# Kernel tuning notes

Measured on AMD Instinct MI355X. Metric: run time of the kernel, lower is better.

## Reference

```python
import jax, jax.numpy as jnp
import numpy as np

B, T, D, H = 2, 2048, 1024, 16
DH = D // H  # head_dim = 64
ROPE_BASE = 10000.0


def _rope_cos_sin(seq_len, dh, dtype):
    inv_freq = 1.0 / (ROPE_BASE ** (jnp.arange(0, dh, 2, dtype=jnp.float32) / dh))
    t = jnp.arange(seq_len, dtype=jnp.float32)
    freqs = jnp.outer(t, inv_freq)            # [T, dh/2]
    emb = jnp.concatenate([freqs, freqs], -1)  # [T, dh]
    return jnp.cos(emb).astype(dtype), jnp.sin(emb).astype(dtype)


def _rotate_half(x):
    half = x.shape[-1] // 2
    return jnp.concatenate([-x[..., half:], x[..., :half]], axis=-1)


def setup_inputs() -> dict:
    key = jax.random.key(0)
    k1, k2, k3 = jax.random.split(key, 3)
    x = jax.random.normal(k1, (B, T, D), dtype=jnp.float32)
    w_qkv = jax.random.normal(k2, (D, 3 * D), dtype=jnp.float32) * (D ** -0.5)
    w_out = jax.random.normal(k3, (D, D), dtype=jnp.float32) * (D ** -0.5)
    return {"x": x, "w_qkv": w_qkv, "w_out": w_out}


def reference(x, w_qkv, w_out):
    b, t, _ = x.shape
    qkv = x @ w_qkv                                        # [B,T,3D]
    qkv = qkv.reshape(b, t, 3, H, DH).transpose(2, 0, 3, 1, 4)  # [3,B,H,T,DH]
    q, k, v = qkv[0], qkv[1], qkv[2]

    cos, sin = _rope_cos_sin(t, DH, x.dtype)               # [T,DH] each
    q = q * cos + _rotate_half(q) * sin
    k = k * cos + _rotate_half(k) * sin

    scale = DH ** -0.5
    scores = jnp.einsum('bhtd,bhsd->bhts', q, k) * scale   # [B,H,T,T]
    # dense additive causal mask (as in original module)
    neg = jnp.finfo(x.dtype).min
    causal = jnp.triu(jnp.ones((t, t), dtype=bool), k=1)
    scores = scores + jnp.where(causal, neg, jnp.zeros((), x.dtype))
    attn = jax.nn.softmax(scores, axis=-1)
    out = jnp.einsum('bhts,bhsd->bhtd', attn, v)           # [B,H,T,DH]
    out = out.transpose(0, 2, 1, 3).reshape(b, t, D)       # [B,T,D]
    return out @ w_out
```

## Files before the change

### kernel.cpp

```cpp
#include <hip/hip_runtime.h>

typedef __bf16 bf16x8 __attribute__((ext_vector_type(8)));
typedef float f32x4 __attribute__((ext_vector_type(4)));
typedef unsigned int u32x4 __attribute__((ext_vector_type(4)));
typedef unsigned int u32x2 __attribute__((ext_vector_type(2)));
typedef unsigned short u16;
typedef unsigned int u32;

#define BSZ 2
#define TSEQ 2048
#define DMODEL 1024
#define NHEAD 16
#define DHEAD 64

#define GLDS(gp, lp)                                                        \
  __builtin_amdgcn_global_load_lds(                                         \
      (const __attribute__((address_space(1))) void*)(gp),                  \
      (__attribute__((address_space(3))) void*)(lp), 16, 0, 0)

#define TRR(dst, base, OFF)                                                 \
  asm volatile("ds_read_b64_tr_b16 %0, %1 offset:" OFF                     \
               : "=v"(dst) : "v"(base) : "memory")

__device__ __forceinline__ u16 f2bf(float f) {
  return __builtin_bit_cast(u16, (__bf16)f);
}
__device__ __forceinline__ float bf2f(u16 h) {
  return __builtin_bit_cast(float, (u32)h << 16);
}

__global__ void k_cvt(const float* __restrict__ in, u16* __restrict__ out, int n4) {
  int i = blockIdx.x * 256 + threadIdx.x;
  if (i >= n4) return;
  float4 v = ((const float4*)in)[i];
  ushort4 o;
  o.x = f2bf(v.x); o.y = f2bf(v.y); o.z = f2bf(v.z); o.w = f2bf(v.w);
  ((ushort4*)out)[i] = o;
}

__global__ void k_transpose_cvt(const float* __restrict__ in, u16* __restrict__ out,
                                int K, int N) {
  __shared__ float tile[64][65];
  int n0 = blockIdx.x * 64, k0 = blockIdx.y * 64;
  int tx = threadIdx.x & 63, ty = threadIdx.x >> 6;
#pragma unroll
  for (int i = ty; i < 64; i += 4)
    tile[i][tx] = in[(size_t)(k0 + i) * N + n0 + tx];
  __syncthreads();
#pragma unroll
  for (int i = ty; i < 64; i += 4)
    out[(size_t)(n0 + i) * K + k0 + tx] = f2bf(tile[tx][i]);
}

__global__ void k_rope_table(float* __restrict__ cosT, float* __restrict__ sinT) {
  int idx = blockIdx.x * 256 + threadIdx.x;
  int t = idx >> 5, f = idx & 31;
  float inv_freq = powf(10000.0f, -(float)(2 * f) / 64.0f);
  float ang = (float)t * inv_freq;
  float s, c;
  sincosf(ang, &s, &c);
  cosT[idx] = c;
  sinT[idx] = s;
}

template <typename OutT>
__global__ __launch_bounds__(256) void k_gemm(const u16* __restrict__ A,
                                              const u16* __restrict__ Bt,
                                              OutT* __restrict__ C, int M, int N, int K) {
  __shared__ __align__(16) u16 a_lds[2][128][32];
  __shared__ __align__(16) u16 b_lds[2][128][32];
  int m0 = blockIdx.y * 128, n0 = blockIdx.x * 128;
  int tid = threadIdx.x;
  int w = tid >> 6, l = tid & 63, lr = l & 15, lg = l >> 4;
  int wr = (w >> 1) * 64, wc = (w & 1) * 64;
  int grow = l >> 2;
  int gcol = (l & 3) * 8;
  f32x4 acc[4][4] = {};

  const u16* a0 = A + (size_t)(m0 + w * 16 + grow) * K + gcol;
  const u16* a1 = A + (size_t)(m0 + (w + 4) * 16 + grow) * K + gcol;
  const u16* b0 = Bt + (size_t)(n0 + w * 16 + grow) * K + gcol;
  const u16* b1 = Bt + (size_t)(n0 + (w + 4) * 16 + grow) * K + gcol;

  int NT = K >> 5;
  GLDS(a0, &a_lds[0][w * 16][0]);
  GLDS(a1, &a_lds[0][(w + 4) * 16][0]);
  GLDS(b0, &b_lds[0][w * 16][0]);
  GLDS(b1, &b_lds[0][(w + 4) * 16][0]);

  for (int t = 0; t < NT; ++t) {
    int p = t & 1;
    if (t + 1 < NT) {
      int k0 = (t + 1) << 5;
      GLDS(a0 + k0, &a_lds[p ^ 1][w * 16][0]);
      GLDS(a1 + k0, &a_lds[p ^ 1][(w + 4) * 16][0]);
      GLDS(b0 + k0, &b_lds[p ^ 1][w * 16][0]);
      GLDS(b1 + k0, &b_lds[p ^ 1][(w + 4) * 16][0]);
      asm volatile("s_waitcnt vmcnt(4)" ::: "memory");
    } else {
      asm volatile("s_waitcnt vmcnt(0)" ::: "memory");
    }
    __builtin_amdgcn_s_barrier();
    __builtin_amdgcn_sched_barrier(0);
    bf16x8 af[4], bfv[4];
#pragma unroll
    for (int mt = 0; mt < 4; ++mt)
      af[mt] = __builtin_bit_cast(bf16x8, *(const u32x4*)&a_lds[p][wr + mt * 16 + lr][lg * 8]);
#pragma unroll
    for (int nt = 0; nt < 4; ++nt)
      bfv[nt] = __builtin_bit_cast(bf16x8, *(const u32x4*)&b_lds[p][wc + nt * 16 + lr][lg * 8]);
    __builtin_amdgcn_s_setprio(1);
#pragma unroll
    for (int mt = 0; mt < 4; ++mt)
#pragma unroll
      for (int nt = 0; nt < 4; ++nt)
        acc[mt][nt] = __builtin_amdgcn_mfma_f32_16x16x32_bf16(af[mt], bfv[nt], acc[mt][nt], 0, 0, 0);
    __builtin_amdgcn_s_setprio(0);
    __builtin_amdgcn_sched_barrier(0);
    __builtin_amdgcn_s_barrier();
  }

#pragma unroll
  for (int mt = 0; mt < 4; ++mt)
#pragma unroll
    for (int nt = 0; nt < 4; ++nt)
#pragma unroll
      for (int r = 0; r < 4; ++r) {
        int row = m0 + wr + mt * 16 + lg * 4 + r;
        int col = n0 + wc + nt * 16 + lr;
        C[(size_t)row * N + col] = acc[mt][nt][r];
      }
}

__global__ __launch_bounds__(256) void k_gemm_qkv(const u16* __restrict__ A,
                                                  const u16* __restrict__ Bt,
                                                  u16* __restrict__ Qh, u16* __restrict__ Kh,
                                                  u16* __restrict__ Vh,
                                                  const float* __restrict__ cosT,
                                                  const float* __restrict__ sinT) {
  const int M = BSZ * TSEQ, N = 3 * DMODEL, K = DMODEL;
  __shared__ __align__(16) u16 a_lds[2][128][32];
  __shared__ __align__(16) u16 b_lds[2][128][32];
  int m0 = blockIdx.y * 128, n0 = blockIdx.x * 128;
  int tid = threadIdx.x;
  int w = tid >> 6, l = tid & 63, lr = l & 15, lg = l >> 4;
  int wr = (w >> 1) * 64, wc = (w & 1) * 64;
  int grow = l >> 2;
  int gcol = (l & 3) * 8;
  f32x4 acc[4][4] = {};

  const u16* a0 = A + (size_t)(m0 + w * 16 + grow) * K + gcol;
  const u16* a1 = A + (size_t)(m0 + (w + 4) * 16 + grow) * K + gcol;
  const u16* b0 = Bt + (size_t)(n0 + w * 16 + grow) * K + gcol;
  const u16* b1 = Bt + (size_t)(n0 + (w + 4) * 16 + grow) * K + gcol;

  int NT = K >> 5;
  GLDS(a0, &a_lds[0][w * 16][0]);
  GLDS(a1, &a_lds[0][(w + 4) * 16][0]);
  GLDS(b0, &b_lds[0][w * 16][0]);
  GLDS(b1, &b_lds[0][(w + 4) * 16][0]);

  for (int t = 0; t < NT; ++t) {
    int p = t & 1;
    if (t + 1 < NT) {
      int k0 = (t + 1) << 5;
      GLDS(a0 + k0, &a_lds[p ^ 1][w * 16][0]);
      GLDS(a1 + k0, &a_lds[p ^ 1][(w + 4) * 16][0]);
      GLDS(b0 + k0, &b_lds[p ^ 1][w * 16][0]);
      GLDS(b1 + k0, &b_lds[p ^ 1][(w + 4) * 16][0]);
      asm volatile("s_waitcnt vmcnt(4)" ::: "memory");
    } else {
      asm volatile("s_waitcnt vmcnt(0)" ::: "memory");
    }
    __builtin_amdgcn_s_barrier();
    __builtin_amdgcn_sched_barrier(0);
    bf16x8 af[4], bfv[4];
#pragma unroll
    for (int mt = 0; mt < 4; ++mt)
      af[mt] = __builtin_bit_cast(bf16x8, *(const u32x4*)&a_lds[p][wr + mt * 16 + lr][lg * 8]);
#pragma unroll
    for (int nt = 0; nt < 4; ++nt)
      bfv[nt] = __builtin_bit_cast(bf16x8, *(const u32x4*)&b_lds[p][wc + nt * 16 + lr][lg * 8]);
    __builtin_amdgcn_s_setprio(1);
#pragma unroll
    for (int mt = 0; mt < 4; ++mt)
#pragma unroll
      for (int nt = 0; nt < 4; ++nt)
        acc[mt][nt] = __builtin_amdgcn_mfma_f32_16x16x32_bf16(af[mt], bfv[nt], acc[mt][nt], 0, 0, 0);
    __builtin_amdgcn_s_setprio(0);
    __builtin_amdgcn_sched_barrier(0);
    __builtin_amdgcn_s_barrier();
  }

  int sec = n0 >> 10;
  int hcol = ((n0 + wc) & 1023) >> 6;
  u16* outp = (sec == 0) ? Qh : (sec == 1) ? Kh : Vh;
  float qscale = (sec == 0) ? 0.125f : 1.0f;
#pragma unroll
  for (int mt = 0; mt < 4; ++mt)
#pragma unroll
    for (int r = 0; r < 4; ++r) {
      int row = m0 + wr + mt * 16 + lg * 4 + r;
      int b = row >> 11, tt = row & 2047;
      size_t obase = ((size_t)((b * 16 + hcol) * 2048 + tt)) * 64;
      if (sec == 2) {
#pragma unroll
        for (int nt = 0; nt < 4; ++nt)
          outp[obase + nt * 16 + lr] = f2bf(acc[mt][nt][r]);
      } else {
        float c0 = cosT[tt * 32 + lr],      s0 = sinT[tt * 32 + lr];
        float c1 = cosT[tt * 32 + 16 + lr], s1 = sinT[tt * 32 + 16 + lr];
        float v0 = acc[mt][0][r], v1 = acc[mt][1][r];
        float v2 = acc[mt][2][r], v3 = acc[mt][3][r];
        outp[obase + lr]      = f2bf((v0 * c0 - v2 * s0) * qscale);
        outp[obase + 16 + lr] = f2bf((v1 * c1 - v3 * s1) * qscale);
        outp[obase + 32 + lr] = f2bf((v2 * c0 + v0 * s0) * qscale);
        outp[obase + 48 + lr] = f2bf((v3 * c1 + v1 * s1) * qscale);
      }
    }
}

__global__ __launch_bounds__(256) void k_flash(const u16* __restrict__ Qg, const u16* __restrict__ Kg,
                                               const u16* __restrict__ Vg, u16* __restrict__ O) {
  __shared__ __align__(16) u16 k_lds[2][64][72];
  __shared__ __align__(16) u16 vsub[2][4096];
  __shared__ __align__(16) u16 p_lds[4][16][68];
  int pairIdx = blockIdx.x;
  int bh = blockIdx.y;
  int b = bh >> 4, h = bh & 15;
  size_t hoff = (size_t)bh * TSEQ * DHEAD;
  int tid = threadIdx.x, w = tid >> 6, l = tid & 63, lr = l & 15, lg = l >> 4;

  int srow = tid >> 3;
  int g8 = tid & 7;
  int sc8 = g8 * 8;
  u32 vtr0 = (u32)(uintptr_t)vsub + (u32)(lg * 1024 + lr * 8);

  const u16* kbase = Kg + hoff;
  const u16* vbase = Vg + hoff;

  for (int sub = 0; sub < 2; ++sub) {
    int qb = sub == 0 ? (31 - pairIdx) : pairIdx;

    int qrow = qb * 64 + w * 16 + lr;
    const u16* qp = Qg + hoff + (size_t)qrow * 64 + lg * 8;
    bf16x8 qf0 = __builtin_bit_cast(bf16x8, *(const u32x4*)qp);
    bf16x8 qf1 = __builtin_bit_cast(bf16x8, *(const u32x4*)(qp + 32));

    f32x4 acc[4] = {};
    float mrow[4] = {-1e30f, -1e30f, -1e30f, -1e30f};
    float lrow[4] = {0.f, 0.f, 0.f, 0.f};

    u32x4 kreg[2], vreg[2];
#pragma unroll
    for (int p = 0; p < 2; ++p) {
      int r = srow + p * 32;
      kreg[p] = *(const u32x4*)(kbase + (size_t)r * 64 + sc8);
      vreg[p] = *(const u32x4*)(vbase + (size_t)r * 64 + sc8);
    }
    __syncthreads();

    for (int kv = 0; kv <= qb; ++kv) {
      int cur = kv & 1;
#pragma unroll
      for (int p = 0; p < 2; ++p) {
        int r = srow + p * 32;
        *(u32x4*)&k_lds[cur][r][sc8] = kreg[p];
        int vo = ((r >> 2) * 4 + (g8 >> 1)) * 64 + (r & 3) * 16 + (g8 & 1) * 8;
        *(u32x4*)&vsub[cur][vo] = vreg[p];
      }
      __syncthreads();
      if (kv < qb) {
#pragma unroll
        for (int p = 0; p < 2; ++p) {
          int r = (kv + 1) * 64 + srow + p * 32;
          kreg[p] = *(const u32x4*)(kbase + (size_t)r * 64 + sc8);
          vreg[p] = *(const u32x4*)(vbase + (size_t)r * 64 + sc8);
        }
      }

      f32x4 s[4];
      __builtin_amdgcn_s_setprio(1);
#pragma unroll
      for (int c = 0; c < 4; ++c) {
        const u16* kp2 = &k_lds[cur][c * 16 + lr][lg * 8];
        bf16x8 kf0 = __builtin_bit_cast(bf16x8, *(const u32x4*)kp2);
        bf16x8 kf1 = __builtin_bit_cast(bf16x8, *(const u32x4*)(kp2 + 32));
        f32x4 z = {};
        z = __builtin_amdgcn_mfma_f32_16x16x32_bf16(qf0, kf0, z, 0, 0, 0);
        s[c] = __builtin_amdgcn_mfma_f32_16x16x32_bf16(qf1, kf1, z, 0, 0, 0);
      }
      __builtin_amdgcn_s_setprio(0);
      if (kv == qb) {
#pragma unroll
        for (int c = 0; c < 4; ++c)
#pragma unroll
          for (int r = 0; r < 4; ++r)
            if (c * 16 + lr > w * 16 + lg * 4 + r) s[c][r] = -1e30f;
      }

      float rmax[4];
#pragma unroll
      for (int r = 0; r < 4; ++r)
        rmax[r] = fmaxf(fmaxf(s[0][r], s[1][r]), fmaxf(s[2][r], s[3][r]));
#pragma unroll
      for (int mset = 1; mset <= 8; mset <<= 1)
#pragma unroll
        for (int r = 0; r < 4; ++r)
          rmax[r] = fmaxf(rmax[r], __shfl_xor(rmax[r], mset, 64));
      bool need = (rmax[0] > mrow[0] + 8.0f) | (rmax[1] > mrow[1] + 8.0f) |
                  (rmax[2] > mrow[2] + 8.0f) | (rmax[3] > mrow[3] + 8.0f);
      if (__any(need)) {
        float alpha[4];
#pragma unroll
        for (int r = 0; r < 4; ++r) {
          float mn = fmaxf(mrow[r], rmax[r]);
          alpha[r] = __expf(mrow[r] - mn);
          mrow[r] = mn;
          lrow[r] *= alpha[r];
        }
#pragma unroll
        for (int n = 0; n < 4; ++n)
#pragma unroll
          for (int r = 0; r < 4; ++r)
            acc[n][r] *= alpha[r];
      }
#pragma unroll
      for (int c = 0; c < 4; ++c)
#pragma unroll
        for (int r = 0; r < 4; ++r) {
          float pe = __expf(s[c][r] - mrow[r]);
          s[c][r] = pe;
          lrow[r] += pe;
        }

#pragma unroll
      for (int c = 0; c < 4; ++c)
#pragma unroll
        for (int r = 0; r < 4; ++r)
          p_lds[w][lg * 4 + r][c * 16 + lr] = f2bf(s[c][r]);
      bf16x8 pa0 = __builtin_bit_cast(bf16x8, *(const u32x4*)&p_lds[w][lr][lg * 8]);
      bf16x8 pa1 = __builtin_bit_cast(bf16x8, *(const u32x4*)&p_lds[w][lr][lg * 8 + 32]);

      u32 vtr = vtr0 + (u32)(cur * 8192);
      {
        u32x2 t[8];
        TRR(t[0], vtr, "0");    TRR(t[1], vtr, "512");
        TRR(t[2], vtr, "4096"); TRR(t[3], vtr, "4608");
        TRR(t[4], vtr, "128");  TRR(t[5], vtr, "640");
        TRR(t[6], vtr, "4224"); TRR(t[7], vtr, "4736");
        asm volatile("s_waitcnt lgkmcnt(0)" ::: "memory");
        __builtin_amdgcn_sched_barrier(0);
        __builtin_amdgcn_s_setprio(1);
#pragma unroll
        for (int n2 = 0; n2 < 2; ++n2) {
          u32x4 vlo, vhi;
          vlo[0] = t[n2 * 4 + 0][0]; vlo[1] = t[n2 * 4 + 0][1];
          vlo[2] = t[n2 * 4 + 1][0]; vlo[3] = t[n2 * 4 + 1][1];
          vhi[0] = t[n2 * 4 + 2][0]; vhi[1] = t[n2 * 4 + 2][1];
          vhi[2] = t[n2 * 4 + 3][0]; vhi[3] = t[n2 * 4 + 3][1];
          acc[n2] = __builtin_amdgcn_mfma_f32_16x16x32_bf16(pa0, __builtin_bit_cast(bf16x8, vlo), acc[n2], 0, 0, 0);
          acc[n2] = __builtin_amdgcn_mfma_f32_16x16x32_bf16(pa1, __builtin_bit_cast(bf16x8, vhi), acc[n2], 0, 0, 0);
        }
        __builtin_amdgcn_s_setprio(0);
      }
      {
        u32x2 t[8];
        TRR(t[0], vtr, "256");  TRR(t[1], vtr, "768");
        TRR(t[2], vtr, "4352"); TRR(t[3], vtr, "4864");
        TRR(t[4], vtr, "384");  TRR(t[5], vtr, "896");
        TRR(t[6], vtr, "4480"); TRR(t[7], vtr, "4992");
        asm volatile("s_waitcnt lgkmcnt(0)" ::: "memory");
        __builtin_amdgcn_sched_barrier(0);
        __builtin_amdgcn_s_setprio(1);
#pragma unroll
        for (int n2 = 0; n2 < 2; ++n2) {
          int n = 2 + n2;
          u32x4 vlo, vhi;
          vlo[0] = t[n2 * 4 + 0][0]; vlo[1] = t[n2 * 4 + 0][1];
          vlo[2] = t[n2 * 4 + 1][0]; vlo[3] = t[n2 * 4 + 1][1];
          vhi[0] = t[n2 * 4 + 2][0]; vhi[1] = t[n2 * 4 + 2][1];
          vhi[2] = t[n2 * 4 + 3][0]; vhi[3] = t[n2 * 4 + 3][1];
          acc[n] = __builtin_amdgcn_mfma_f32_16x16x32_bf16(pa0, __builtin_bit_cast(bf16x8, vlo), acc[n], 0, 0, 0);
          acc[n] = __builtin_amdgcn_mfma_f32_16x16x32_bf16(pa1, __builtin_bit_cast(bf16x8, vhi), acc[n], 0, 0, 0);
        }
        __builtin_amdgcn_s_setprio(0);
      }
    }

#pragma unroll
    for (int mset = 1; mset <= 8; mset <<= 1)
#pragma unroll
      for (int r = 0; r < 4; ++r)
        lrow[r] += __shfl_xor(lrow[r], mset, 64);
#pragma unroll
    for (int n = 0; n < 4; ++n)
#pragma unroll
      for (int r = 0; r < 4; ++r) {
        int t = qb * 64 + w * 16 + lg * 4 + r;
        int dd = n * 16 + lr;
        float ov = acc[n][r] / lrow[r];
        O[(size_t)(b * TSEQ + t) * DMODEL + h * 64 + dd] = f2bf(ov);
      }
  }
}

extern "C" void kernel_launch(void* const* d_in, const int* in_sizes, int n_in,
                              void* d_out, int out_size, void* d_ws, size_t ws_size,
                              hipStream_t stream) {
  const float* x     = (const float*)d_in[0];
  const float* w_qkv = (const float*)d_in[1];
  const float* w_out = (const float*)d_in[2];
  float* out = (float*)d_out;

  char* ws = (char*)d_ws;
  size_t off = 0;
  auto alloc = [&](size_t bytes) {
    char* p = ws + off;
    off += (bytes + 255) & ~(size_t)255;
    return p;
  };
  const size_t MT = (size_t)BSZ * TSEQ;
  u16* xb    = (u16*)alloc(MT * DMODEL * 2);
  u16* wqkvT = (u16*)alloc((size_t)3 * DMODEL * DMODEL * 2);
  u16* woutT = (u16*)alloc((size_t)DMODEL * DMODEL * 2);
  u16* Qh    = (u16*)alloc(MT * DMODEL * 2);
  u16* Kh    = (u16*)alloc(MT * DMODEL * 2);
  u16* Vh    = (u16*)alloc(MT * DMODEL * 2);
  u16* aout  = (u16*)alloc(MT * DMODEL * 2);
  float* cosT = (float*)alloc((size_t)TSEQ * 32 * 4);
  float* sinT = (float*)alloc((size_t)TSEQ * 32 * 4);
  if (ws_size < off) return;

  k_cvt<<<(MT * DMODEL / 4 + 255) / 256, 256, 0, stream>>>(x, xb, MT * DMODEL / 4);
  k_transpose_cvt<<<dim3(48, 16), 256, 0, stream>>>(w_qkv, wqkvT, DMODEL, 3 * DMODEL);
  k_transpose_cvt<<<dim3(16, 16), 256, 0, stream>>>(w_out, woutT, DMODEL, DMODEL);
  k_rope_table<<<(TSEQ * 32) / 256, 256, 0, stream>>>(cosT, sinT);
  k_gemm_qkv<<<dim3(24, 32), 256, 0, stream>>>(xb, wqkvT, Qh, Kh, Vh, cosT, sinT);
  k_flash<<<dim3(16, BSZ * NHEAD), 256, 0, stream>>>(Qh, Kh, Vh, aout);
  k_gemm<float><<<dim3(8, 32), 256, 0, stream>>>(aout, woutT, out, (int)MT, DMODEL, DMODEL);
}
```

Measured before the change: 218.2 us.

## Merge prep kernels, run both causal query blocks concurrently, shrink output GEMM tile

The four preprocessing kernels (x convert, two weight transposes, rope table) are merged into one launch to cut launch overhead. The flash kernel now uses 512 threads, with two 4-wave teams each handling one query block of the balanced pair at the same time over a shared K/V stream, instead of processing the pair one after the other. The output projection gets its own kernel with 128x64 tiles, doubling the number of blocks so the GPU is better filled. Costs: more LDS and registers per flash block, and the team with the shorter query block sits idle during the later KV iterations while still joining the barriers.

```diff
diff --git a/kernel.cpp b/kernel.cpp
--- a/kernel.cpp
+++ b/kernel.cpp
@@ -25,48 +25,68 @@
 __device__ __forceinline__ u16 f2bf(float f) {
   return __builtin_bit_cast(u16, (__bf16)f);
 }
+__device__ __forceinline__ u32 pack2bf(float lo, float hi) {
+  return (u32)f2bf(lo) | ((u32)f2bf(hi) << 16);
+}
 __device__ __forceinline__ float bf2f(u16 h) {
   return __builtin_bit_cast(float, (u32)h << 16);
 }
 
-__global__ void k_cvt(const float* __restrict__ in, u16* __restrict__ out, int n4) {
-  int i = blockIdx.x * 256 + threadIdx.x;
-  if (i >= n4) return;
-  float4 v = ((const float4*)in)[i];
-  ushort4 o;
-  o.x = f2bf(v.x); o.y = f2bf(v.y); o.z = f2bf(v.z); o.w = f2bf(v.w);
-  ((ushort4*)out)[i] = o;
-}
-
-__global__ void k_transpose_cvt(const float* __restrict__ in, u16* __restrict__ out,
-                                int K, int N) {
+__global__ void k_prep(const float* __restrict__ x, u16* __restrict__ xb,
+                       const float* __restrict__ wqkv, u16* __restrict__ wqkvT,
+                       const float* __restrict__ wout, u16* __restrict__ woutT,
+                       float* __restrict__ cosT, float* __restrict__ sinT) {
   __shared__ float tile[64][65];
-  int n0 = blockIdx.x * 64, k0 = blockIdx.y * 64;
-  int tx = threadIdx.x & 63, ty = threadIdx.x >> 6;
-#pragma unroll
-  for (int i = ty; i < 64; i += 4)
-    tile[i][tx] = in[(size_t)(k0 + i) * N + n0 + tx];
-  __syncthreads();
-#pragma unroll
-  for (int i = ty; i < 64; i += 4)
-    out[(size_t)(n0 + i) * K + k0 + tx] = f2bf(tile[tx][i]);
-}
-
-__global__ void k_rope_table(float* __restrict__ cosT, float* __restrict__ sinT) {
-  int idx = blockIdx.x * 256 + threadIdx.x;
-  int t = idx >> 5, f = idx & 31;
-  float inv_freq = powf(10000.0f, -(float)(2 * f) / 64.0f);
-  float ang = (float)t * inv_freq;
-  float s, c;
-  sincosf(ang, &s, &c);
-  cosT[idx] = c;
-  sinT[idx] = s;
-}
-
-template <typename OutT>
-__global__ __launch_bounds__(256) void k_gemm(const u16* __restrict__ A,
-                                              const u16* __restrict__ Bt,
-                                              OutT* __restrict__ C, int M, int N, int K) {
+  int blk = blockIdx.x, tid = threadIdx.x;
+  if (blk < 2048) {
+    int i = blk * 256 + tid;
+    const float4* f4 = (const float4*)x;
+    float4 v0 = f4[i * 2], v1 = f4[i * 2 + 1];
+    u32x4 o;
+    o[0] = pack2bf(v0.x, v0.y); o[1] = pack2bf(v0.z, v0.w);
+    o[2] = pack2bf(v1.x, v1.y); o[3] = pack2bf(v1.z, v1.w);
+    ((u32x4*)xb)[i] = o;
+  } else if (blk < 2816) {
+    int idx = blk - 2048;
+    int n0 = (idx % 48) * 64, k0 = (idx / 48) * 64;
+    int tx = tid & 63, ty = tid >> 6;
+#pragma unroll
+    for (int i = ty; i < 64; i += 4)
+      tile[i][tx] = wqkv[(size_t)(k0 + i) * 3072 + n0 + tx];
+    __syncthreads();
+#pragma unroll
+    for (int i = ty; i < 64; i += 4)
+      wqkvT[(size_t)(n0 + i) * 1024 + k0 + tx] = f2bf(tile[tx][i]);
+  } else if (blk < 3072) {
+    int idx = blk - 2816;
+    int n0 = (idx % 16) * 64, k0 = (idx / 16) * 64;
+    int tx = tid & 63, ty = tid >> 6;
+#pragma unroll
+    for (int i = ty; i < 64; i += 4)
+      tile[i][tx] = wout[(size_t)(k0 + i) * 1024 + n0 + tx];
+    __syncthreads();
+#pragma unroll
+    for (int i = ty; i < 64; i += 4)
+      woutT[(size_t)(n0 + i) * 1024 + k0 + tx] = f2bf(tile[tx][i]);
+  } else {
+    int idx = (blk - 3072) * 256 + tid;
+    int t = idx >> 5, f = idx & 31;
+    float inv_freq = powf(10000.0f, -(float)(2 * f) / 64.0f);
+    float ang = (float)t * inv_freq;
+    float s, c;
+    sincosf(ang, &s, &c);
+    cosT[idx] = c;
+    sinT[idx] = s;
+  }
+}
+
+__global__ __launch_bounds__(256) void k_gemm_qkv(const u16* __restrict__ A,
+                                                  const u16* __restrict__ Bt,
+                                                  u16* __restrict__ Qh, u16* __restrict__ Kh,
+                                                  u16* __restrict__ Vh,
+                                                  const float* __restrict__ cosT,
+                                                  const float* __restrict__ sinT) {
+  const int K = DMODEL;
   __shared__ __align__(16) u16 a_lds[2][128][32];
   __shared__ __align__(16) u16 b_lds[2][128][32];
   int m0 = blockIdx.y * 128, n0 = blockIdx.x * 128;
@@ -120,78 +140,6 @@
     __builtin_amdgcn_s_barrier();
   }
 
-#pragma unroll
-  for (int mt = 0; mt < 4; ++mt)
-#pragma unroll
-    for (int nt = 0; nt < 4; ++nt)
-#pragma unroll
-      for (int r = 0; r < 4; ++r) {
-        int row = m0 + wr + mt * 16 + lg * 4 + r;
-        int col = n0 + wc + nt * 16 + lr;
-        C[(size_t)row * N + col] = acc[mt][nt][r];
-      }
-}
-
-__global__ __launch_bounds__(256) void k_gemm_qkv(const u16* __restrict__ A,
-                                                  const u16* __restrict__ Bt,
-                                                  u16* __restrict__ Qh, u16* __restrict__ Kh,
-                                                  u16* __restrict__ Vh,
-                                                  const float* __restrict__ cosT,
-                                                  const float* __restrict__ sinT) {
-  const int M = BSZ * TSEQ, N = 3 * DMODEL, K = DMODEL;
-  __shared__ __align__(16) u16 a_lds[2][128][32];
-  __shared__ __align__(16) u16 b_lds[2][128][32];
-  int m0 = blockIdx.y * 128, n0 = blockIdx.x * 128;
-  int tid = threadIdx.x;
-  int w = tid >> 6, l = tid & 63, lr = l & 15, lg = l >> 4;
-  int wr = (w >> 1) * 64, wc = (w & 1) * 64;
-  int grow = l >> 2;
-  int gcol = (l & 3) * 8;
-  f32x4 acc[4][4] = {};
-
-  const u16* a0 = A + (size_t)(m0 + w * 16 + grow) * K + gcol;
-  const u16* a1 = A + (size_t)(m0 + (w + 4) * 16 + grow) * K + gcol;
-  const u16* b0 = Bt + (size_t)(n0 + w * 16 + grow) * K + gcol;
-  const u16* b1 = Bt + (size_t)(n0 + (w + 4) * 16 + grow) * K + gcol;
-
-  int NT = K >> 5;
-  GLDS(a0, &a_lds[0][w * 16][0]);
-  GLDS(a1, &a_lds[0][(w + 4) * 16][0]);
-  GLDS(b0, &b_lds[0][w * 16][0]);
-  GLDS(b1, &b_lds[0][(w + 4) * 16][0]);
-
-  for (int t = 0; t < NT; ++t) {
-    int p = t & 1;
-    if (t + 1 < NT) {
-      int k0 = (t + 1) << 5;
-      GLDS(a0 + k0, &a_lds[p ^ 1][w * 16][0]);
-      GLDS(a1 + k0, &a_lds[p ^ 1][(w + 4) * 16][0]);
-      GLDS(b0 + k0, &b_lds[p ^ 1][w * 16][0]);
-      GLDS(b1 + k0, &b_lds[p ^ 1][(w + 4) * 16][0]);
-      asm volatile("s_waitcnt vmcnt(4)" ::: "memory");
-    } else {
-      asm volatile("s_waitcnt vmcnt(0)" ::: "memory");
-    }
-    __builtin_amdgcn_s_barrier();
-    __builtin_amdgcn_sched_barrier(0);
-    bf16x8 af[4], bfv[4];
-#pragma unroll
-    for (int mt = 0; mt < 4; ++mt)
-      af[mt] = __builtin_bit_cast(bf16x8, *(const u32x4*)&a_lds[p][wr + mt * 16 + lr][lg * 8]);
-#pragma unroll
-    for (int nt = 0; nt < 4; ++nt)
-      bfv[nt] = __builtin_bit_cast(bf16x8, *(const u32x4*)&b_lds[p][wc + nt * 16 + lr][lg * 8]);
-    __builtin_amdgcn_s_setprio(1);
-#pragma unroll
-    for (int mt = 0; mt < 4; ++mt)
-#pragma unroll
-      for (int nt = 0; nt < 4; ++nt)
-        acc[mt][nt] = __builtin_amdgcn_mfma_f32_16x16x32_bf16(af[mt], bfv[nt], acc[mt][nt], 0, 0, 0);
-    __builtin_amdgcn_s_setprio(0);
-    __builtin_amdgcn_sched_barrier(0);
-    __builtin_amdgcn_s_barrier();
-  }
-
   int sec = n0 >> 10;
   int hcol = ((n0 + wc) & 1023) >> 6;
   u16* outp = (sec == 0) ? Qh : (sec == 1) ? Kh : Vh;
@@ -220,16 +168,85 @@
     }
 }
 
-__global__ __launch_bounds__(256) void k_flash(const u16* __restrict__ Qg, const u16* __restrict__ Kg,
+__global__ __launch_bounds__(256) void k_gemm_out(const u16* __restrict__ A,
+                                                  const u16* __restrict__ Bt,
+                                                  float* __restrict__ C) {
+  const int N = 1024, K = 1024;
+  __shared__ __align__(16) u16 a_lds[2][128][32];
+  __shared__ __align__(16) u16 b_lds[2][64][32];
+  int m0 = blockIdx.y * 128, n0 = blockIdx.x * 64;
+  int tid = threadIdx.x;
+  int w = tid >> 6, l = tid & 63, lr = l & 15, lg = l >> 4;
+  int wr = (w >> 1) * 64, wc = (w & 1) * 32;
+  int grow = l >> 2;
+  int gcol = (l & 3) * 8;
+  f32x4 acc[4][2] = {};
+
+  const u16* a0 = A + (size_t)(m0 + w * 16 + grow) * K + gcol;
+  const u16* a1 = A + (size_t)(m0 + (w + 4) * 16 + grow) * K + gcol;
+  const u16* b0 = Bt + (size_t)(n0 + w * 16 + grow) * K + gcol;
+
+  int NT = K >> 5;
+  GLDS(a0, &a_lds[0][w * 16][0]);
+  GLDS(a1, &a_lds[0][(w + 4) * 16][0]);
+  GLDS(b0, &b_lds[0][w * 16][0]);
+
+  for (int t = 0; t < NT; ++t) {
+    int p = t & 1;
+    if (t + 1 < NT) {
+      int k0 = (t + 1) << 5;
+      GLDS(a0 + k0, &a_lds[p ^ 1][w * 16][0]);
+      GLDS(a1 + k0, &a_lds[p ^ 1][(w + 4) * 16][0]);
+      GLDS(b0 + k0, &b_lds[p ^ 1][w * 16][0]);
+      asm volatile("s_waitcnt vmcnt(3)" ::: "memory");
+    } else {
+      asm volatile("s_waitcnt vmcnt(0)" ::: "memory");
+    }
+    __builtin_amdgcn_s_barrier();
+    __builtin_amdgcn_sched_barrier(0);
+    bf16x8 af[4], bfv[2];
+#pragma unroll
+    for (int mt = 0; mt < 4; ++mt)
+      af[mt] = __builtin_bit_cast(bf16x8, *(const u32x4*)&a_lds[p][wr + mt * 16 + lr][lg * 8]);
+#pragma unroll
+    for (int nt = 0; nt < 2; ++nt)
+      bfv[nt] = __builtin_bit_cast(bf16x8, *(const u32x4*)&b_lds[p][wc + nt * 16 + lr][lg * 8]);
+    __builtin_amdgcn_s_setprio(1);
+#pragma unroll
+    for (int mt = 0; mt < 4; ++mt)
+#pragma unroll
+      for (int nt = 0; nt < 2; ++nt)
+        acc[mt][nt] = __builtin_amdgcn_mfma_f32_16x16x32_bf16(af[mt], bfv[nt], acc[mt][nt], 0, 0, 0);
+    __builtin_amdgcn_s_setprio(0);
+    __builtin_amdgcn_sched_barrier(0);
+    __builtin_amdgcn_s_barrier();
+  }
+
+#pragma unroll
+  for (int mt = 0; mt < 4; ++mt)
+#pragma unroll
+    for (int nt = 0; nt < 2; ++nt)
+#pragma unroll
+      for (int r = 0; r < 4; ++r) {
+        int row = m0 + wr + mt * 16 + lg * 4 + r;
+        int col = n0 + wc + nt * 16 + lr;
+        C[(size_t)row * N + col] = acc[mt][nt][r];
+      }
+}
+
+__global__ __launch_bounds__(512) void k_flash(const u16* __restrict__ Qg, const u16* __restrict__ Kg,
                                                const u16* __restrict__ Vg, u16* __restrict__ O) {
   __shared__ __align__(16) u16 k_lds[2][64][72];
   __shared__ __align__(16) u16 vsub[2][4096];
-  __shared__ __align__(16) u16 p_lds[4][16][68];
-  int pairIdx = blockIdx.x;
+  __shared__ __align__(16) u16 p_lds[8][16][68];
+  int pp = blockIdx.x;
+  int qb1 = 31 - pp, qb2 = pp;
   int bh = blockIdx.y;
   int b = bh >> 4, h = bh & 15;
   size_t hoff = (size_t)bh * TSEQ * DHEAD;
   int tid = threadIdx.x, w = tid >> 6, l = tid & 63, lr = l & 15, lg = l >> 4;
+  int team = w >> 2, wt = w & 3;
+  int qb_t = team ? qb2 : qb1;
 
   int srow = tid >> 3;
   int g8 = tid & 7;
@@ -239,46 +256,32 @@
   const u16* kbase = Kg + hoff;
   const u16* vbase = Vg + hoff;
 
-  for (int sub = 0; sub < 2; ++sub) {
-    int qb = sub == 0 ? (31 - pairIdx) : pairIdx;
-
-    int qrow = qb * 64 + w * 16 + lr;
-    const u16* qp = Qg + hoff + (size_t)qrow * 64 + lg * 8;
-    bf16x8 qf0 = __builtin_bit_cast(bf16x8, *(const u32x4*)qp);
-    bf16x8 qf1 = __builtin_bit_cast(bf16x8, *(const u32x4*)(qp + 32));
-
-    f32x4 acc[4] = {};
-    float mrow[4] = {-1e30f, -1e30f, -1e30f, -1e30f};
-    float lrow[4] = {0.f, 0.f, 0.f, 0.f};
-
-    u32x4 kreg[2], vreg[2];
-#pragma unroll
-    for (int p = 0; p < 2; ++p) {
-      int r = srow + p * 32;
-      kreg[p] = *(const u32x4*)(kbase + (size_t)r * 64 + sc8);
-      vreg[p] = *(const u32x4*)(vbase + (size_t)r * 64 + sc8);
-    }
+  const u16* qp = Qg + hoff + (size_t)(qb_t * 64 + wt * 16 + lr) * 64 + lg * 8;
+  bf16x8 qf0 = __builtin_bit_cast(bf16x8, *(const u32x4*)qp);
+  bf16x8 qf1 = __builtin_bit_cast(bf16x8, *(const u32x4*)(qp + 32));
+
+  f32x4 acc[4] = {};
+  float mrow[4] = {-1e30f, -1e30f, -1e30f, -1e30f};
+  float lsum[4] = {0.f, 0.f, 0.f, 0.f};
+
+  u32x4 kreg, vreg;
+  kreg = *(const u32x4*)(kbase + (size_t)srow * 64 + sc8);
+  vreg = *(const u32x4*)(vbase + (size_t)srow * 64 + sc8);
+
+  for (int kv = 0; kv <= qb1; ++kv) {
+    int cur = kv & 1;
+    *(u32x4*)&k_lds[cur][srow][sc8] = kreg;
+    int vo = ((srow >> 2) * 4 + (g8 >> 1)) * 64 + (srow & 3) * 16 + (g8 & 1) * 8;
+    *(u32x4*)&vsub[cur][vo] = vreg;
     __syncthreads();
-
-    for (int kv = 0; kv <= qb; ++kv) {
-      int cur = kv & 1;
-#pragma unroll
-      for (int p = 0; p < 2; ++p) {
-        int r = srow + p * 32;
-        *(u32x4*)&k_lds[cur][r][sc8] = kreg[p];
-        int vo = ((r >> 2) * 4 + (g8 >> 1)) * 64 + (r & 3) * 16 + (g8 & 1) * 8;
-        *(u32x4*)&vsub[cur][vo] = vreg[p];
-      }
-      __syncthreads();
-      if (kv < qb) {
-#pragma unroll
-        for (int p = 0; p < 2; ++p) {
-          int r = (kv + 1) * 64 + srow + p * 32;
-          kreg[p] = *(const u32x4*)(kbase + (size_t)r * 64 + sc8);
-          vreg[p] = *(const u32x4*)(vbase + (size_t)r * 64 + sc8);
-        }
-      }
-
+    if (kv < qb1) {
+      int r = (kv + 1) * 64 + srow;
+      kreg = *(const u32x4*)(kbase + (size_t)r * 64 + sc8);
+      vreg = *(const u32x4*)(vbase + (size_t)r * 64 + sc8);
+    }
+
+    if (kv <= qb_t) {
+      u32 vtr = vtr0 + (u32)(cur * 8192);
       f32x4 s[4];
       __builtin_amdgcn_s_setprio(1);
 #pragma unroll
@@ -291,12 +294,12 @@
         s[c] = __builtin_amdgcn_mfma_f32_16x16x32_bf16(qf1, kf1, z, 0, 0, 0);
       }
       __builtin_amdgcn_s_setprio(0);
-      if (kv == qb) {
+      if (kv == qb_t) {
 #pragma unroll
         for (int c = 0; c < 4; ++c)
 #pragma unroll
           for (int r = 0; r < 4; ++r)
-            if (c * 16 + lr > w * 16 + lg * 4 + r) s[c][r] = -1e30f;
+            if (c * 16 + lr > wt * 16 + lg * 4 + r) s[c][r] = -1e30f;
       }
 
       float rmax[4];
@@ -317,7 +320,7 @@
           float mn = fmaxf(mrow[r], rmax[r]);
           alpha[r] = __expf(mrow[r] - mn);
           mrow[r] = mn;
-          lrow[r] *= alpha[r];
+          lsum[r] *= alpha[r];
         }
 #pragma unroll
         for (int n = 0; n < 4; ++n)
@@ -331,7 +334,7 @@
         for (int r = 0; r < 4; ++r) {
           float pe = __expf(s[c][r] - mrow[r]);
           s[c][r] = pe;
-          lrow[r] += pe;
+          lsum[r] += pe;
         }
 
 #pragma unroll
@@ -342,7 +345,6 @@
       bf16x8 pa0 = __builtin_bit_cast(bf16x8, *(const u32x4*)&p_lds[w][lr][lg * 8]);
       bf16x8 pa1 = __builtin_bit_cast(bf16x8, *(const u32x4*)&p_lds[w][lr][lg * 8 + 32]);
 
-      u32 vtr = vtr0 + (u32)(cur * 8192);
       {
         u32x2 t[8];
         TRR(t[0], vtr, "0");    TRR(t[1], vtr, "512");
@@ -387,22 +389,21 @@
         __builtin_amdgcn_s_setprio(0);
       }
     }
-
-#pragma unroll
-    for (int mset = 1; mset <= 8; mset <<= 1)
-#pragma unroll
-      for (int r = 0; r < 4; ++r)
-        lrow[r] += __shfl_xor(lrow[r], mset, 64);
-#pragma unroll
-    for (int n = 0; n < 4; ++n)
-#pragma unroll
-      for (int r = 0; r < 4; ++r) {
-        int t = qb * 64 + w * 16 + lg * 4 + r;
-        int dd = n * 16 + lr;
-        float ov = acc[n][r] / lrow[r];
-        O[(size_t)(b * TSEQ + t) * DMODEL + h * 64 + dd] = f2bf(ov);
-      }
   }
+
+#pragma unroll
+  for (int mset = 1; mset <= 8; mset <<= 1)
+#pragma unroll
+    for (int r = 0; r < 4; ++r)
+      lsum[r] += __shfl_xor(lsum[r], mset, 64);
+#pragma unroll
+  for (int n = 0; n < 4; ++n)
+#pragma unroll
+    for (int r = 0; r < 4; ++r) {
+      int t = qb_t * 64 + wt * 16 + lg * 4 + r;
+      int dd = n * 16 + lr;
+      O[(size_t)(b * TSEQ + t) * DMODEL + h * 64 + dd] = f2bf(acc[n][r] / lsum[r]);
+    }
 }
 
 extern "C" void kernel_launch(void* const* d_in, const int* in_sizes, int n_in,
@@ -432,11 +433,8 @@
   float* sinT = (float*)alloc((size_t)TSEQ * 32 * 4);
   if (ws_size < off) return;
 
-  k_cvt<<<(MT * DMODEL / 4 + 255) / 256, 256, 0, stream>>>(x, xb, MT * DMODEL / 4);
-  k_transpose_cvt<<<dim3(48, 16), 256, 0, stream>>>(w_qkv, wqkvT, DMODEL, 3 * DMODEL);
-  k_transpose_cvt<<<dim3(16, 16), 256, 0, stream>>>(w_out, woutT, DMODEL, DMODEL);
-  k_rope_table<<<(TSEQ * 32) / 256, 256, 0, stream>>>(cosT, sinT);
+  k_prep<<<3328, 256, 0, stream>>>(x, xb, w_qkv, wqkvT, w_out, woutT, cosT, sinT);
   k_gemm_qkv<<<dim3(24, 32), 256, 0, stream>>>(xb, wqkvT, Qh, Kh, Vh, cosT, sinT);
-  k_flash<<<dim3(16, BSZ * NHEAD), 256, 0, stream>>>(Qh, Kh, Vh, aout);
-  k_gemm<float><<<dim3(8, 32), 256, 0, stream>>>(aout, woutT, out, (int)MT, DMODEL, DMODEL);
-}
+  k_flash<<<dim3(16, BSZ * NHEAD), 512, 0, stream>>>(Qh, Kh, Vh, aout);
+  k_gemm_out<<<dim3(16, 32), 256, 0, stream>>>(aout, woutT, out);
+}
```

Result: faster. 199.3 us (-8.6%).
